# Optimization experiments

Hardware: AMD Instinct MI355X
Metric: run time of the kernel (lower is better)

Reference implementation:

```python
import jax, jax.numpy as jnp
import numpy as np

B, S = 4, 1024
IN_F, OUT_F = 8192, 8192
ACT_BITS = 8


def setup_inputs() -> dict:
    key = jax.random.key(0)
    k1, k2, k3, k4 = jax.random.split(key, 4)
    x = jax.random.normal(k1, (B, S, IN_F), dtype=jnp.float32)
    # each int8 byte packs two 4-bit exponent nibbles; stored as int32 values in [0, 256)
    packed_exponents = jax.random.randint(k2, (OUT_F, IN_F // 2), 0, 256, dtype=jnp.int32)
    # signs are +/-1 per weight element
    signs = jax.random.randint(k3, (OUT_F, IN_F), 0, 2, dtype=jnp.int32) * 2 - 1
    bias = jax.random.normal(k4, (OUT_F,), dtype=jnp.float32)
    activation_scale = jnp.float32(0.02)  # delta_lsb for int8 activation quant
    min_exp = -14  # python int constant (buffer min_exp in the torch module)
    return {
        "x": x,
        "packed_exponents": packed_exponents,
        "signs": signs,
        "bias": bias,
        "activation_scale": activation_scale,
        "min_exp": min_exp,
    }


def reference(x, packed_exponents, signs, bias, activation_scale, min_exp):
    q_max = 2 ** (ACT_BITS - 1) - 1   # 127
    q_min = -2 ** (ACT_BITS - 1)      # -128
    orig_shape = x.shape
    x2 = x.reshape(-1, orig_shape[-1])  # [N, IN_F]

    # int8 activation quantization (kept in float; values are exact small ints)
    a_quant = jnp.clip(jnp.round(x2 / activation_scale), q_min, q_max)

    # unpack two 4-bit exponent nibbles per byte: low nibble first, then high
    lo = packed_exponents & 0xF
    hi = (packed_exponents >> 4) & 0xF
    exps = jnp.stack([lo, hi], axis=-1).reshape(OUT_F, IN_F)  # [OUT_F, IN_F]

    # dequantized log-domain weights: sign * 2^(nibble + min_exp)
    w = signs.astype(jnp.float32) * jnp.exp2((exps + min_exp).astype(jnp.float32))

    # batched matvec (the CUDA kernel does one row of this per launch) + dequant + bias
    out = (a_quant @ w.T) * activation_scale + bias  # [N, OUT_F]
    return out.reshape(*orig_shape[:-1], OUT_F)
```

## Files before the change

### kernel.cpp

```cpp
#include <hip/hip_runtime.h>
#include <hip/hip_bf16.h>
#include <stdint.h>

#define N_TOK 4096
#define KF    8192
#define NF    8192

#define BM 256
#define BN 256
#define NT (KF / 64)
#define NKH (KF / 32)

typedef __attribute__((ext_vector_type(8))) short short8;
typedef __attribute__((ext_vector_type(4))) float f32x4;

#define GLOBAL_P(p) ((const __attribute__((address_space(1))) void*)(p))
#define LDS_P(p)    ((__attribute__((address_space(3))) void*)(p))

__global__ void quant_x(const float* __restrict__ x, const float* __restrict__ scale_p,
                        uint16_t* __restrict__ a) {
    const float s = *scale_p;
    const int n8 = N_TOK * KF / 8;
    const int stride = gridDim.x * blockDim.x;
    for (int i = blockIdx.x * blockDim.x + threadIdx.x; i < n8; i += stride) {
        const float4* xp = (const float4*)(x + (size_t)i * 8);
        float4 v0 = xp[0], v1 = xp[1];
        float q[8] = {v0.x, v0.y, v0.z, v0.w, v1.x, v1.y, v1.z, v1.w};
        union { uint16_t u16[8]; short8 v; } o;
        #pragma unroll
        for (int j = 0; j < 8; ++j) {
            float t = rintf(q[j] / s);
            t = fminf(fmaxf(t, -128.f), 127.f);
            union { float f; uint32_t u; } cv; cv.f = t;
            o.u16[j] = (uint16_t)(cv.u >> 16);
        }
        *(short8*)(a + (size_t)i * 8) = o.v;
    }
}

__global__ void dequant_w(const int* __restrict__ packed, const int* __restrict__ signs,
                          const int* __restrict__ minexp_p, uint16_t* __restrict__ w) {
    const int me = *minexp_p;
    const int ebase = (me + 127) << 7;
    const int n4 = NF * (KF / 2) / 4;
    const int stride = gridDim.x * blockDim.x;
    for (int i = blockIdx.x * blockDim.x + threadIdx.x; i < n4; i += stride) {
        int4 p  = ((const int4*)packed)[i];
        int4 s0 = ((const int4*)signs)[(size_t)i * 2];
        int4 s1 = ((const int4*)signs)[(size_t)i * 2 + 1];
        int pw[4] = {p.x, p.y, p.z, p.w};
        int sg[8] = {s0.x, s0.y, s0.z, s0.w, s1.x, s1.y, s1.z, s1.w};
        union { uint16_t u16[8]; short8 v; } o;
        #pragma unroll
        for (int j = 0; j < 4; ++j) {
            int lo = pw[j] & 0xF, hi = (pw[j] >> 4) & 0xF;
            o.u16[2 * j]     = (uint16_t)((ebase + (lo << 7)) | (sg[2 * j]     < 0 ? 0x8000 : 0));
            o.u16[2 * j + 1] = (uint16_t)((ebase + (hi << 7)) | (sg[2 * j + 1] < 0 ? 0x8000 : 0));
        }
        *(short8*)(w + (size_t)i * 8) = o.v;
    }
}

#define BARRIER()  __builtin_amdgcn_s_barrier()
#define SCHED0()   __builtin_amdgcn_sched_barrier(0)
#define WAITVM8()  do { asm volatile("s_waitcnt vmcnt(8)"); SCHED0(); } while (0)
#define WAITVM4()  do { asm volatile("s_waitcnt vmcnt(4)"); SCHED0(); } while (0)
#define WAITVM0()  do { asm volatile("s_waitcnt vmcnt(0)"); SCHED0(); } while (0)
#define SP1 __builtin_amdgcn_s_setprio(1)
#define SP0 __builtin_amdgcn_s_setprio(0)

__global__ __launch_bounds__(512, 2) void gemm_bt(
        const uint16_t* __restrict__ A, const uint16_t* __restrict__ W,
        const float* __restrict__ bias, const float* __restrict__ scale_p,
        float* __restrict__ out) {
    __shared__ uint16_t ldsA[4 * 256 * 32];
    __shared__ uint16_t ldsB[4 * 256 * 32];

    const int tid  = threadIdx.x;
    const int wid  = tid >> 6, lane = tid & 63;
    const int wr = wid >> 2, wc = wid & 3;
    const int rlane = lane & 15, kgrp = lane >> 4;

    const int bid = blockIdx.x;
    const int xcd = bid & 7;
    const int i_l = bid >> 3;
    const int gen = i_l >> 5;
    const int il  = i_l & 31;
    const int by  = gen * 8 + (il >> 2);
    const int bx  = xcd * 4 + (il & 3);
    const int rowA0 = by * BM;
    const int colB0 = bx * BN;

    const int o0 = tid * 16, o1 = (512 + tid) * 16;
    const int l0 = o0 ^ (((o0 >> 9) & 1) << 5);
    const int l1 = o1 ^ (((o1 >> 9) & 1) << 5);
    const char* gA0 = (const char*)A + ((size_t)(rowA0 + (l0 >> 6)) * KF) * 2 + (l0 & 63);
    const char* gA1 = (const char*)A + ((size_t)(rowA0 + (l1 >> 6)) * KF) * 2 + (l1 & 63);
    const char* gB0 = (const char*)W + ((size_t)(colB0 + (l0 >> 6)) * KF) * 2 + (l0 & 63);
    const char* gB1 = (const char*)W + ((size_t)(colB0 + (l1 >> 6)) * KF) * 2 + (l1 & 63);
    const int ldst0 = wid * 1024;
    const int ldst1 = 8192 + wid * 1024;

    int aoff[8], boff[4];
    #pragma unroll
    for (int i = 0; i < 8; ++i) {
        int row = wr * 128 + i * 16 + rlane;
        int o = row * 64 + kgrp * 16;
        aoff[i] = o ^ (((o >> 9) & 1) << 5);
    }
    #pragma unroll
    for (int n = 0; n < 4; ++n) {
        int row = wc * 64 + n * 16 + rlane;
        int o = row * 64 + kgrp * 16;
        boff[n] = o ^ (((o >> 9) & 1) << 5);
    }

#define STAGE_A(j) do { \
    char* b_ = (char*)ldsA + ((j) & 3) * 16384; \
    __builtin_amdgcn_global_load_lds(GLOBAL_P(gA0 + (size_t)(j) * 64), LDS_P(b_ + ldst0), 16, 0, 0); \
    __builtin_amdgcn_global_load_lds(GLOBAL_P(gA1 + (size_t)(j) * 64), LDS_P(b_ + ldst1), 16, 0, 0); \
} while (0)
#define STAGE_B(j) do { \
    char* b_ = (char*)ldsB + ((j) & 3) * 16384; \
    __builtin_amdgcn_global_load_lds(GLOBAL_P(gB0 + (size_t)(j) * 64), LDS_P(b_ + ldst0), 16, 0, 0); \
    __builtin_amdgcn_global_load_lds(GLOBAL_P(gB1 + (size_t)(j) * 64), LDS_P(b_ + ldst1), 16, 0, 0); \
} while (0)
#define LDA4(DST, H, SLOT) do { \
    const char* p_ = (const char*)ldsA + (SLOT) * 16384; \
    _Pragma("unroll") for (int i_ = 0; i_ < 4; ++i_) \
        DST[i_] = *(const short8*)(p_ + aoff[(H) * 4 + i_]); \
} while (0)
#define LDB4(DST, SLOT) do { \
    const char* p_ = (const char*)ldsB + (SLOT) * 16384; \
    _Pragma("unroll") for (int i_ = 0; i_ < 4; ++i_) \
        DST[i_] = *(const short8*)(p_ + boff[i_]); \
} while (0)
#define MFMA16(H, AF, BF) do { \
    SP1; \
    _Pragma("unroll") for (int mm_ = 0; mm_ < 4; ++mm_) \
        _Pragma("unroll") for (int nn_ = 0; nn_ < 4; ++nn_) \
            acc[(H) * 4 + mm_][nn_] = __builtin_amdgcn_mfma_f32_16x16x32_bf16( \
                AF[mm_], BF[nn_], acc[(H) * 4 + mm_][nn_], 0, 0, 0); \
    SP0; \
} while (0)

#define TILE(S0, S1, S0N, ST0, ST1, ST2, ST3, VM0, VM2) do { \
    BARRIER(); VM0; LDA4(afrY, 1, S0);                 ST0; MFMA16(0, afrX, bfrE); \
    BARRIER();      LDA4(afrX, 0, S1); LDB4(bfrO, S1); ST1; MFMA16(1, afrY, bfrE); \
    BARRIER(); VM2; LDA4(afrY, 1, S1);                 ST2; MFMA16(0, afrX, bfrO); \
    BARRIER();      LDA4(afrX, 0, S0N); LDB4(bfrE, S0N); ST3; MFMA16(1, afrY, bfrO); \
} while (0)

    f32x4 acc[8][4] = {};
    short8 afrX[4], afrY[4], bfrE[4], bfrO[4];

    STAGE_A(0); STAGE_B(0);
    STAGE_A(1); STAGE_B(1);
    STAGE_A(2); STAGE_B(2);
    WAITVM8();
    BARRIER();
    LDA4(afrX, 0, 0);
    LDB4(bfrE, 0);

    for (int kt2 = 0; kt2 < 63; ++kt2) {
        const int j0 = kt2 * 4;
        TILE(0, 1, 2,
             STAGE_A(j0 + 3), STAGE_B(j0 + 3), STAGE_A(j0 + 4), STAGE_B(j0 + 4),
             WAITVM4(), WAITVM4());
        TILE(2, 3, 0,
             STAGE_A(j0 + 5), STAGE_B(j0 + 5), STAGE_A(j0 + 6), STAGE_B(j0 + 6),
             WAITVM4(), WAITVM4());
    }

    TILE(0, 1, 2,
         STAGE_A(255), STAGE_B(255), (void)0, (void)0,
         WAITVM4(), WAITVM4());

    BARRIER(); WAITVM0(); LDA4(afrY, 1, 2); MFMA16(0, afrX, bfrE);
    BARRIER(); LDA4(afrX, 0, 3); LDB4(bfrO, 3); MFMA16(1, afrY, bfrE);
    BARRIER(); LDA4(afrY, 1, 3); MFMA16(0, afrX, bfrO);
    BARRIER(); MFMA16(1, afrY, bfrO);

    const float s = *scale_p;
    const int colbase = colB0 + wc * 64 + rlane;
    const int rowbase = rowA0 + wr * 128 + kgrp * 4;
    #pragma unroll
    for (int n = 0; n < 4; ++n) {
        const float bv = bias[colbase + n * 16];
        #pragma unroll
        for (int mf = 0; mf < 8; ++mf) {
            #pragma unroll
            for (int r = 0; r < 4; ++r)
                out[(size_t)(rowbase + mf * 16 + r) * NF + colbase + n * 16] = acc[mf][n][r] * s + bv;
        }
    }
#undef STAGE_A
#undef STAGE_B
#undef LDA4
#undef LDB4
#undef MFMA16
#undef TILE
}

extern "C" void kernel_launch(void* const* d_in, const int* in_sizes, int n_in,
                              void* d_out, int out_size, void* d_ws, size_t ws_size,
                              hipStream_t stream) {
    const float* x      = (const float*)d_in[0];
    const int*   packed = (const int*)d_in[1];
    const int*   signs  = (const int*)d_in[2];
    const float* bias   = (const float*)d_in[3];
    const float* scale  = (const float*)d_in[4];
    const int*   minexp = (const int*)d_in[5];
    float* out = (float*)d_out;

    uint16_t* A = (uint16_t*)d_ws;
    uint16_t* W = (uint16_t*)((char*)d_ws + (size_t)N_TOK * KF * 2);

    quant_x<<<2048, 256, 0, stream>>>(x, scale, A);
    dequant_w<<<2048, 256, 0, stream>>>(packed, signs, minexp, W);
    gemm_bt<<<(N_TOK / BM) * (NF / BN), 512, 0, stream>>>(A, W, bias, scale, out);
}
```

Measured before the change: 615.3 us.

## Replace register double-buffered fragments with single-buffer, barrier-synchronized K-loop schedule

Removes the ping-pong register fragments (afrX/afrY, bfrE/bfrO) that overlapped LDS reads with MFMAs. Each half-tile now loads its A/B fragments from LDS, waits on lgkmcnt(0) behind a barrier, then runs its MFMAs, with global-to-LDS staging interleaved. This cuts VGPR pressure and simplifies the schedule, but serializes LDS reads against matrix math and adds barriers, which can expose LDS latency.

```diff
diff --git a/kernel.cpp b/kernel.cpp
--- a/kernel.cpp
+++ b/kernel.cpp
@@ -9,7 +9,6 @@
 #define BM 256
 #define BN 256
 #define NT (KF / 64)
-#define NKH (KF / 32)
 
 typedef __attribute__((ext_vector_type(8))) short short8;
 typedef __attribute__((ext_vector_type(4))) float f32x4;
@@ -63,6 +62,7 @@
 
 #define BARRIER()  __builtin_amdgcn_s_barrier()
 #define SCHED0()   __builtin_amdgcn_sched_barrier(0)
+#define LGKM0()    do { asm volatile("s_waitcnt lgkmcnt(0)"); SCHED0(); } while (0)
 #define WAITVM8()  do { asm volatile("s_waitcnt vmcnt(8)"); SCHED0(); } while (0)
 #define WAITVM4()  do { asm volatile("s_waitcnt vmcnt(4)"); SCHED0(); } while (0)
 #define WAITVM0()  do { asm volatile("s_waitcnt vmcnt(0)"); SCHED0(); } while (0)
@@ -125,61 +125,92 @@
     __builtin_amdgcn_global_load_lds(GLOBAL_P(gB0 + (size_t)(j) * 64), LDS_P(b_ + ldst0), 16, 0, 0); \
     __builtin_amdgcn_global_load_lds(GLOBAL_P(gB1 + (size_t)(j) * 64), LDS_P(b_ + ldst1), 16, 0, 0); \
 } while (0)
-#define LDA4(DST, H, SLOT) do { \
+#define LDA4(H, SLOT) do { \
     const char* p_ = (const char*)ldsA + (SLOT) * 16384; \
     _Pragma("unroll") for (int i_ = 0; i_ < 4; ++i_) \
-        DST[i_] = *(const short8*)(p_ + aoff[(H) * 4 + i_]); \
-} while (0)
-#define LDB4(DST, SLOT) do { \
+        afr[i_] = *(const short8*)(p_ + aoff[(H) * 4 + i_]); \
+} while (0)
+#define LDB4(SLOT) do { \
     const char* p_ = (const char*)ldsB + (SLOT) * 16384; \
     _Pragma("unroll") for (int i_ = 0; i_ < 4; ++i_) \
-        DST[i_] = *(const short8*)(p_ + boff[i_]); \
-} while (0)
-#define MFMA16(H, AF, BF) do { \
+        bfr[i_] = *(const short8*)(p_ + boff[i_]); \
+} while (0)
+#define MFMA16(H) do { \
     SP1; \
     _Pragma("unroll") for (int mm_ = 0; mm_ < 4; ++mm_) \
         _Pragma("unroll") for (int nn_ = 0; nn_ < 4; ++nn_) \
             acc[(H) * 4 + mm_][nn_] = __builtin_amdgcn_mfma_f32_16x16x32_bf16( \
-                AF[mm_], BF[nn_], acc[(H) * 4 + mm_][nn_], 0, 0, 0); \
+                afr[mm_], bfr[nn_], acc[(H) * 4 + mm_][nn_], 0, 0, 0); \
     SP0; \
 } while (0)
 
-#define TILE(S0, S1, S0N, ST0, ST1, ST2, ST3, VM0, VM2) do { \
-    BARRIER(); VM0; LDA4(afrY, 1, S0);                 ST0; MFMA16(0, afrX, bfrE); \
-    BARRIER();      LDA4(afrX, 0, S1); LDB4(bfrO, S1); ST1; MFMA16(1, afrY, bfrE); \
-    BARRIER(); VM2; LDA4(afrY, 1, S1);                 ST2; MFMA16(0, afrX, bfrO); \
-    BARRIER();      LDA4(afrX, 0, S0N); LDB4(bfrE, S0N); ST3; MFMA16(1, afrY, bfrO); \
-} while (0)
-
     f32x4 acc[8][4] = {};
-    short8 afrX[4], afrY[4], bfrE[4], bfrO[4];
+    short8 afr[4], bfr[4];
 
     STAGE_A(0); STAGE_B(0);
     STAGE_A(1); STAGE_B(1);
     STAGE_A(2); STAGE_B(2);
     WAITVM8();
     BARRIER();
-    LDA4(afrX, 0, 0);
-    LDB4(bfrE, 0);
-
-    for (int kt2 = 0; kt2 < 63; ++kt2) {
-        const int j0 = kt2 * 4;
-        TILE(0, 1, 2,
-             STAGE_A(j0 + 3), STAGE_B(j0 + 3), STAGE_A(j0 + 4), STAGE_B(j0 + 4),
-             WAITVM4(), WAITVM4());
-        TILE(2, 3, 0,
-             STAGE_A(j0 + 5), STAGE_B(j0 + 5), STAGE_A(j0 + 6), STAGE_B(j0 + 6),
-             WAITVM4(), WAITVM4());
-    }
-
-    TILE(0, 1, 2,
-         STAGE_A(255), STAGE_B(255), (void)0, (void)0,
-         WAITVM4(), WAITVM4());
-
-    BARRIER(); WAITVM0(); LDA4(afrY, 1, 2); MFMA16(0, afrX, bfrE);
-    BARRIER(); LDA4(afrX, 0, 3); LDB4(bfrO, 3); MFMA16(1, afrY, bfrE);
-    BARRIER(); LDA4(afrY, 1, 3); MFMA16(0, afrX, bfrO);
-    BARRIER(); MFMA16(1, afrY, bfrO);
+
+    for (int t = 0; t < 126; ++t) {
+        const int j0 = 2 * t;
+        const int s0 = j0 & 3, s1 = (j0 + 1) & 3;
+        LDA4(0, s0); LDB4(s0); STAGE_A(j0 + 3);
+        BARRIER(); LGKM0();
+        MFMA16(0);
+        BARRIER();
+        LDA4(1, s0); STAGE_B(j0 + 3);
+        BARRIER(); LGKM0();
+        MFMA16(1);
+        WAITVM8();
+        BARRIER();
+        LDA4(0, s1); LDB4(s1); STAGE_A(j0 + 4);
+        BARRIER(); LGKM0();
+        MFMA16(0);
+        BARRIER();
+        LDA4(1, s1); STAGE_B(j0 + 4);
+        BARRIER(); LGKM0();
+        MFMA16(1);
+        WAITVM8();
+        BARRIER();
+    }
+
+    LDA4(0, 0); LDB4(0); STAGE_A(255);
+    BARRIER(); LGKM0();
+    MFMA16(0);
+    BARRIER();
+    LDA4(1, 0); STAGE_B(255);
+    BARRIER(); LGKM0();
+    MFMA16(1);
+    WAITVM8();
+    BARRIER();
+    LDA4(0, 1); LDB4(1);
+    BARRIER(); LGKM0();
+    MFMA16(0);
+    BARRIER();
+    LDA4(1, 1);
+    BARRIER(); LGKM0();
+    MFMA16(1);
+    WAITVM4();
+    BARRIER();
+
+    LDA4(0, 2); LDB4(2);
+    BARRIER(); LGKM0();
+    MFMA16(0);
+    BARRIER();
+    LDA4(1, 2);
+    BARRIER(); LGKM0();
+    MFMA16(1);
+    WAITVM0();
+    BARRIER();
+    LDA4(0, 3); LDB4(3);
+    BARRIER(); LGKM0();
+    MFMA16(0);
+    BARRIER();
+    LDA4(1, 3);
+    LGKM0();
+    MFMA16(1);
 
     const float s = *scale_p;
     const int colbase = colB0 + wc * 64 + rlane;
@@ -199,7 +230,6 @@
 #undef LDA4
 #undef LDB4
 #undef MFMA16
-#undef TILE
 }
 
 extern "C" void kernel_launch(void* const* d_in, const int* in_sizes, int n_in,
```

After: 681.2 us. 1.11x slower.

## Restructure GEMM main loop into one-barrier-per-k-tile windows with split staging

Applied to the files above, without the earlier changes.

Replaces the four-barrier-per-two-k-tile schedule with a window that issues one barrier per k-tile and interleaves LDS fragment loads, async global-to-LDS staging of A and B, and two MFMA half-blocks. The wait for outstanding loads moves to the end of each window. The aim is to cut barrier stalls and overlap LDS reads with MFMA work more evenly. The cost is tighter slot-reuse hazards in the 4-deep ring buffer, which could race if the vmcnt and barrier placement is off.

```diff
diff --git a/kernel.cpp b/kernel.cpp
--- a/kernel.cpp
+++ b/kernel.cpp
@@ -8,8 +8,6 @@
 
 #define BM 256
 #define BN 256
-#define NT (KF / 64)
-#define NKH (KF / 32)
 
 typedef __attribute__((ext_vector_type(8))) short short8;
 typedef __attribute__((ext_vector_type(4))) float f32x4;
@@ -63,7 +61,6 @@
 
 #define BARRIER()  __builtin_amdgcn_s_barrier()
 #define SCHED0()   __builtin_amdgcn_sched_barrier(0)
-#define WAITVM8()  do { asm volatile("s_waitcnt vmcnt(8)"); SCHED0(); } while (0)
 #define WAITVM4()  do { asm volatile("s_waitcnt vmcnt(4)"); SCHED0(); } while (0)
 #define WAITVM0()  do { asm volatile("s_waitcnt vmcnt(0)"); SCHED0(); } while (0)
 #define SP1 __builtin_amdgcn_s_setprio(1)
@@ -125,7 +122,7 @@
     __builtin_amdgcn_global_load_lds(GLOBAL_P(gB0 + (size_t)(j) * 64), LDS_P(b_ + ldst0), 16, 0, 0); \
     __builtin_amdgcn_global_load_lds(GLOBAL_P(gB1 + (size_t)(j) * 64), LDS_P(b_ + ldst1), 16, 0, 0); \
 } while (0)
-#define LDA4(DST, H, SLOT) do { \
+#define LDAH(DST, H, SLOT) do { \
     const char* p_ = (const char*)ldsA + (SLOT) * 16384; \
     _Pragma("unroll") for (int i_ = 0; i_ < 4; ++i_) \
         DST[i_] = *(const short8*)(p_ + aoff[(H) * 4 + i_]); \
@@ -135,51 +132,62 @@
     _Pragma("unroll") for (int i_ = 0; i_ < 4; ++i_) \
         DST[i_] = *(const short8*)(p_ + boff[i_]); \
 } while (0)
-#define MFMA16(H, AF, BF) do { \
+#define MFMAH(H, A4, B4) do { \
     SP1; \
     _Pragma("unroll") for (int mm_ = 0; mm_ < 4; ++mm_) \
         _Pragma("unroll") for (int nn_ = 0; nn_ < 4; ++nn_) \
             acc[(H) * 4 + mm_][nn_] = __builtin_amdgcn_mfma_f32_16x16x32_bf16( \
-                AF[mm_], BF[nn_], acc[(H) * 4 + mm_][nn_], 0, 0, 0); \
+                A4[mm_], B4[nn_], acc[(H) * 4 + mm_][nn_], 0, 0, 0); \
     SP0; \
 } while (0)
 
-#define TILE(S0, S1, S0N, ST0, ST1, ST2, ST3, VM0, VM2) do { \
-    BARRIER(); VM0; LDA4(afrY, 1, S0);                 ST0; MFMA16(0, afrX, bfrE); \
-    BARRIER();      LDA4(afrX, 0, S1); LDB4(bfrO, S1); ST1; MFMA16(1, afrY, bfrE); \
-    BARRIER(); VM2; LDA4(afrY, 1, S1);                 ST2; MFMA16(0, afrX, bfrO); \
-    BARRIER();      LDA4(afrX, 0, S0N); LDB4(bfrE, S0N); ST3; MFMA16(1, afrY, bfrO); \
+#define WINDOW(BC, BN_, SC, SN, JST, VM) do { \
+    BARRIER(); \
+    LDAH(aQ, 1, SC);             \
+    STAGE_A(JST); \
+    MFMAH(0, aP, BC); \
+    LDAH(aP, 0, SN);             \
+    LDB4(BN_, SN);               \
+    STAGE_B(JST); \
+    MFMAH(1, aQ, BC); \
+    VM; \
+} while (0)
+#define WINDOW_NS(BC, BN_, SC, SN, VM) do { \
+    BARRIER(); \
+    LDAH(aQ, 1, SC); \
+    MFMAH(0, aP, BC); \
+    LDAH(aP, 0, SN); \
+    LDB4(BN_, SN); \
+    MFMAH(1, aQ, BC); \
+    VM; \
 } while (0)
 
     f32x4 acc[8][4] = {};
-    short8 afrX[4], afrY[4], bfrE[4], bfrO[4];
+    short8 aP[4], aQ[4], bP[4], bQ[4];
 
     STAGE_A(0); STAGE_B(0);
     STAGE_A(1); STAGE_B(1);
     STAGE_A(2); STAGE_B(2);
-    WAITVM8();
+    WAITVM4();
     BARRIER();
-    LDA4(afrX, 0, 0);
-    LDB4(bfrE, 0);
-
-    for (int kt2 = 0; kt2 < 63; ++kt2) {
-        const int j0 = kt2 * 4;
-        TILE(0, 1, 2,
-             STAGE_A(j0 + 3), STAGE_B(j0 + 3), STAGE_A(j0 + 4), STAGE_B(j0 + 4),
-             WAITVM4(), WAITVM4());
-        TILE(2, 3, 0,
-             STAGE_A(j0 + 5), STAGE_B(j0 + 5), STAGE_A(j0 + 6), STAGE_B(j0 + 6),
-             WAITVM4(), WAITVM4());
-    }
-
-    TILE(0, 1, 2,
-         STAGE_A(255), STAGE_B(255), (void)0, (void)0,
-         WAITVM4(), WAITVM4());
-
-    BARRIER(); WAITVM0(); LDA4(afrY, 1, 2); MFMA16(0, afrX, bfrE);
-    BARRIER(); LDA4(afrX, 0, 3); LDB4(bfrO, 3); MFMA16(1, afrY, bfrE);
-    BARRIER(); LDA4(afrY, 1, 3); MFMA16(0, afrX, bfrO);
-    BARRIER(); MFMA16(1, afrY, bfrO);
+    LDAH(aP, 0, 0);
+    LDB4(bP, 0);
+
+    for (int kt = 0; kt < 63; ++kt) {
+        const int j0 = 4 * kt;
+        WINDOW(bP, bQ, 0, 1, j0 + 3, WAITVM4());
+        WINDOW(bQ, bP, 1, 2, j0 + 4, WAITVM4());
+        WINDOW(bP, bQ, 2, 3, j0 + 5, WAITVM4());
+        WINDOW(bQ, bP, 3, 0, j0 + 6, WAITVM4());
+    }
+
+    WINDOW(bP, bQ, 0, 1, 255, WAITVM4());
+    WINDOW_NS(bQ, bP, 1, 2, WAITVM0());
+    WINDOW_NS(bP, bQ, 2, 3, (void)0);
+    BARRIER();
+    LDAH(aQ, 1, 3);
+    MFMAH(0, aP, bQ);
+    MFMAH(1, aQ, bQ);
 
     const float s = *scale_p;
     const int colbase = colB0 + wc * 64 + rlane;
@@ -196,10 +204,11 @@
     }
 #undef STAGE_A
 #undef STAGE_B
-#undef LDA4
+#undef LDAH
 #undef LDB4
-#undef MFMA16
-#undef TILE
+#undef MFMAH
+#undef WINDOW
+#undef WINDOW_NS
 }
 
 extern "C" void kernel_launch(void* const* d_in, const int* in_sizes, int n_in,
```

Result: no change. 604.2 us (-1.8%).

## Shrink GEMM tile to 256x128 with 4 waves and double-buffered LDS

Applied to the files above, without the earlier changes.

Changes the bf16 GEMM block tile from 256x256 with 8 waves to 256x128 with 4 waves. The LDS ring drops from 4 stages to 2, and the pipeline is simplified to a single-stage prefetch with a full vmcnt(0) wait each K step. The block-to-tile mapping is also reworked for XCD locality. The aim is to raise occupancy and shrink LDS per block. In exchange it halves operand reuse per block and exposes more global-load latency, since less prefetch depth is in flight.

```diff
diff --git a/kernel.cpp b/kernel.cpp
--- a/kernel.cpp
+++ b/kernel.cpp
@@ -7,9 +7,7 @@
 #define NF    8192
 
 #define BM 256
-#define BN 256
-#define NT (KF / 64)
-#define NKH (KF / 32)
+#define BN 128
 
 typedef __attribute__((ext_vector_type(8))) short short8;
 typedef __attribute__((ext_vector_type(4))) float f32x4;
@@ -63,43 +61,43 @@
 
 #define BARRIER()  __builtin_amdgcn_s_barrier()
 #define SCHED0()   __builtin_amdgcn_sched_barrier(0)
-#define WAITVM8()  do { asm volatile("s_waitcnt vmcnt(8)"); SCHED0(); } while (0)
-#define WAITVM4()  do { asm volatile("s_waitcnt vmcnt(4)"); SCHED0(); } while (0)
 #define WAITVM0()  do { asm volatile("s_waitcnt vmcnt(0)"); SCHED0(); } while (0)
 #define SP1 __builtin_amdgcn_s_setprio(1)
 #define SP0 __builtin_amdgcn_s_setprio(0)
 
-__global__ __launch_bounds__(512, 2) void gemm_bt(
+__global__ __launch_bounds__(256, 2) void gemm_bt(
         const uint16_t* __restrict__ A, const uint16_t* __restrict__ W,
         const float* __restrict__ bias, const float* __restrict__ scale_p,
         float* __restrict__ out) {
-    __shared__ uint16_t ldsA[4 * 256 * 32];
-    __shared__ uint16_t ldsB[4 * 256 * 32];
+    __shared__ uint16_t ldsA[2 * 256 * 32];
+    __shared__ uint16_t ldsB[2 * 128 * 32];
 
     const int tid  = threadIdx.x;
     const int wid  = tid >> 6, lane = tid & 63;
-    const int wr = wid >> 2, wc = wid & 3;
+    const int wr = wid >> 1, wc = wid & 1;
     const int rlane = lane & 15, kgrp = lane >> 4;
 
     const int bid = blockIdx.x;
     const int xcd = bid & 7;
-    const int i_l = bid >> 3;
-    const int gen = i_l >> 5;
-    const int il  = i_l & 31;
-    const int by  = gen * 8 + (il >> 2);
-    const int bx  = xcd * 4 + (il & 3);
+    const int i_g = bid >> 3;
+    const int gen = i_g >> 5;
+    const int il  = i_g & 31;
+    const int by  = il >> 1;
+    const int bx  = xcd * 8 + gen * 2 + (il & 1);
     const int rowA0 = by * BM;
     const int colB0 = bx * BN;
 
-    const int o0 = tid * 16, o1 = (512 + tid) * 16;
-    const int l0 = o0 ^ (((o0 >> 9) & 1) << 5);
-    const int l1 = o1 ^ (((o1 >> 9) & 1) << 5);
-    const char* gA0 = (const char*)A + ((size_t)(rowA0 + (l0 >> 6)) * KF) * 2 + (l0 & 63);
-    const char* gA1 = (const char*)A + ((size_t)(rowA0 + (l1 >> 6)) * KF) * 2 + (l1 & 63);
-    const char* gB0 = (const char*)W + ((size_t)(colB0 + (l0 >> 6)) * KF) * 2 + (l0 & 63);
-    const char* gB1 = (const char*)W + ((size_t)(colB0 + (l1 >> 6)) * KF) * 2 + (l1 & 63);
-    const int ldst0 = wid * 1024;
-    const int ldst1 = 8192 + wid * 1024;
+    const char* gA[4];
+    const char* gB[2];
+    #pragma unroll
+    for (int q = 0; q < 4; ++q) {
+        int o = (q * 256 + tid) * 16;
+        int l = o ^ (((o >> 9) & 1) << 5);
+        gA[q] = (const char*)A + (size_t)(rowA0 + (l >> 6)) * (KF * 2) + (l & 63);
+        if (q < 2)
+            gB[q] = (const char*)W + (size_t)(colB0 + (l >> 6)) * (KF * 2) + (l & 63);
+    }
+    const int ldst = wid * 1024;
 
     int aoff[8], boff[4];
     #pragma unroll
@@ -116,14 +114,16 @@
     }
 
 #define STAGE_A(j) do { \
-    char* b_ = (char*)ldsA + ((j) & 3) * 16384; \
-    __builtin_amdgcn_global_load_lds(GLOBAL_P(gA0 + (size_t)(j) * 64), LDS_P(b_ + ldst0), 16, 0, 0); \
-    __builtin_amdgcn_global_load_lds(GLOBAL_P(gA1 + (size_t)(j) * 64), LDS_P(b_ + ldst1), 16, 0, 0); \
+    char* b_ = (char*)ldsA + ((j) & 1) * 16384; \
+    _Pragma("unroll") for (int q_ = 0; q_ < 4; ++q_) \
+        __builtin_amdgcn_global_load_lds(GLOBAL_P(gA[q_] + (size_t)(j) * 64), \
+                                         LDS_P(b_ + q_ * 4096 + ldst), 16, 0, 0); \
 } while (0)
 #define STAGE_B(j) do { \
-    char* b_ = (char*)ldsB + ((j) & 3) * 16384; \
-    __builtin_amdgcn_global_load_lds(GLOBAL_P(gB0 + (size_t)(j) * 64), LDS_P(b_ + ldst0), 16, 0, 0); \
-    __builtin_amdgcn_global_load_lds(GLOBAL_P(gB1 + (size_t)(j) * 64), LDS_P(b_ + ldst1), 16, 0, 0); \
+    char* b_ = (char*)ldsB + ((j) & 1) * 8192; \
+    _Pragma("unroll") for (int q_ = 0; q_ < 2; ++q_) \
+        __builtin_amdgcn_global_load_lds(GLOBAL_P(gB[q_] + (size_t)(j) * 64), \
+                                         LDS_P(b_ + q_ * 4096 + ldst), 16, 0, 0); \
 } while (0)
 #define LDA4(DST, H, SLOT) do { \
     const char* p_ = (const char*)ldsA + (SLOT) * 16384; \
@@ -131,55 +131,46 @@
         DST[i_] = *(const short8*)(p_ + aoff[(H) * 4 + i_]); \
 } while (0)
 #define LDB4(DST, SLOT) do { \
-    const char* p_ = (const char*)ldsB + (SLOT) * 16384; \
+    const char* p_ = (const char*)ldsB + (SLOT) * 8192; \
     _Pragma("unroll") for (int i_ = 0; i_ < 4; ++i_) \
         DST[i_] = *(const short8*)(p_ + boff[i_]); \
 } while (0)
-#define MFMA16(H, AF, BF) do { \
+#define MFMAH(H, A4, B4) do { \
     SP1; \
     _Pragma("unroll") for (int mm_ = 0; mm_ < 4; ++mm_) \
         _Pragma("unroll") for (int nn_ = 0; nn_ < 4; ++nn_) \
             acc[(H) * 4 + mm_][nn_] = __builtin_amdgcn_mfma_f32_16x16x32_bf16( \
-                AF[mm_], BF[nn_], acc[(H) * 4 + mm_][nn_], 0, 0, 0); \
+                A4[mm_], B4[nn_], acc[(H) * 4 + mm_][nn_], 0, 0, 0); \
     SP0; \
 } while (0)
 
-#define TILE(S0, S1, S0N, ST0, ST1, ST2, ST3, VM0, VM2) do { \
-    BARRIER(); VM0; LDA4(afrY, 1, S0);                 ST0; MFMA16(0, afrX, bfrE); \
-    BARRIER();      LDA4(afrX, 0, S1); LDB4(bfrO, S1); ST1; MFMA16(1, afrY, bfrE); \
-    BARRIER(); VM2; LDA4(afrY, 1, S1);                 ST2; MFMA16(0, afrX, bfrO); \
-    BARRIER();      LDA4(afrX, 0, S0N); LDB4(bfrE, S0N); ST3; MFMA16(1, afrY, bfrO); \
+#define WINDOW(SC, JST) do { \
+    BARRIER(); \
+    STAGE_A(JST); STAGE_B(JST); \
+    LDB4(bf, SC); LDA4(af, 0, SC); \
+    MFMAH(0, af, bf); \
+    LDA4(ag, 1, SC); \
+    MFMAH(1, ag, bf); \
+    WAITVM0(); \
 } while (0)
 
     f32x4 acc[8][4] = {};
-    short8 afrX[4], afrY[4], bfrE[4], bfrO[4];
+    short8 af[4], ag[4], bf[4];
 
     STAGE_A(0); STAGE_B(0);
-    STAGE_A(1); STAGE_B(1);
-    STAGE_A(2); STAGE_B(2);
-    WAITVM8();
+    WAITVM0();
+
+    for (int kt = 0; kt < 127; ++kt) {
+        WINDOW(0, 2 * kt + 1);
+        WINDOW(1, 2 * kt + 2);
+    }
+    WINDOW(0, 255);
+
     BARRIER();
-    LDA4(afrX, 0, 0);
-    LDB4(bfrE, 0);
-
-    for (int kt2 = 0; kt2 < 63; ++kt2) {
-        const int j0 = kt2 * 4;
-        TILE(0, 1, 2,
-             STAGE_A(j0 + 3), STAGE_B(j0 + 3), STAGE_A(j0 + 4), STAGE_B(j0 + 4),
-             WAITVM4(), WAITVM4());
-        TILE(2, 3, 0,
-             STAGE_A(j0 + 5), STAGE_B(j0 + 5), STAGE_A(j0 + 6), STAGE_B(j0 + 6),
-             WAITVM4(), WAITVM4());
-    }
-
-    TILE(0, 1, 2,
-         STAGE_A(255), STAGE_B(255), (void)0, (void)0,
-         WAITVM4(), WAITVM4());
-
-    BARRIER(); WAITVM0(); LDA4(afrY, 1, 2); MFMA16(0, afrX, bfrE);
-    BARRIER(); LDA4(afrX, 0, 3); LDB4(bfrO, 3); MFMA16(1, afrY, bfrE);
-    BARRIER(); LDA4(afrY, 1, 3); MFMA16(0, afrX, bfrO);
-    BARRIER(); MFMA16(1, afrY, bfrO);
+    LDB4(bf, 1); LDA4(af, 0, 1);
+    MFMAH(0, af, bf);
+    LDA4(ag, 1, 1);
+    MFMAH(1, ag, bf);
 
     const float s = *scale_p;
     const int colbase = colB0 + wc * 64 + rlane;
@@ -198,8 +189,8 @@
 #undef STAGE_B
 #undef LDA4
 #undef LDB4
-#undef MFMA16
-#undef TILE
+#undef MFMAH
+#undef WINDOW
 }
 
 extern "C" void kernel_launch(void* const* d_in, const int* in_sizes, int n_in,
@@ -218,5 +209,5 @@
 
     quant_x<<<2048, 256, 0, stream>>>(x, scale, A);
     dequant_w<<<2048, 256, 0, stream>>>(packed, signs, minexp, W);
-    gemm_bt<<<(N_TOK / BM) * (NF / BN), 512, 0, stream>>>(A, W, bias, scale, out);
-}
+    gemm_bt<<<(N_TOK / BM) * (NF / BN), 256, 0, stream>>>(A, W, bias, scale, out);
+}
```

Result: slower. 803.9 us (+30.6%).
